# Performance work log

Measured on AMD Instinct MI355X. Metric: run time of the kernel, lower is better.

## Reference

```python
import jax, jax.numpy as jnp
import numpy as np

B, C_IN, T = 32, 192, 8192
H, N_PH, OUT = 192, 1024, 4
EPS = 1e-5


def setup_inputs() -> dict:
    key = jax.random.key(0)
    ks = jax.random.split(key, 12)
    s = 0.02
    return {
        "x": jax.random.normal(ks[0], (B, C_IN, T), jnp.float32),
        "x_mask": jnp.ones((B, 1, N_PH), jnp.float32),
        "w": jax.random.randint(ks[1], (B, 1, N_PH), 0, 8, jnp.int32),
        "pre_w": jax.random.normal(ks[2], (H, C_IN), jnp.float32) * s,
        "pre_b": jnp.zeros((H,), jnp.float32),
        "conv0_w": jax.random.normal(ks[3], (H, H, 3), jnp.float32) * s,
        "conv0_b": jnp.zeros((H,), jnp.float32),
        "ln0_g": jnp.ones((H,), jnp.float32),
        "ln0_b": jnp.zeros((H,), jnp.float32),
        "conv1_w": jax.random.normal(ks[4], (H, H, 3), jnp.float32) * s,
        "conv1_b": jnp.zeros((H,), jnp.float32),
        "ln1_g": jnp.ones((H,), jnp.float32),
        "ln1_b": jnp.zeros((H,), jnp.float32),
        "lin_w": jax.random.normal(ks[5], (OUT, H), jnp.float32) * s,
        "lin_b": jnp.zeros((OUT,), jnp.float32),
    }


def _segment_mean(x, w2):
    # x: [B, C, T] frames; w2: [B, n_ph] int durations.
    # Faithful to the torch double loop: phoneme j pools frames
    # [cumsum(w)[j-1] : cumsum(w)[j]); w==0 -> zeros.
    ends = jnp.cumsum(w2, axis=1)                      # [B, n_ph]
    t = jnp.arange(x.shape[2], dtype=ends.dtype)       # [T]
    ph_id = jax.vmap(lambda e: jnp.searchsorted(e, t, side="right"))(ends)  # [B, T]
    # segment sums over frames; extra segment n_ph catches out-of-range frames
    sums = jax.vmap(lambda xt, ids: jax.ops.segment_sum(xt, ids, num_segments=N_PH + 1))(
        x.transpose(0, 2, 1), ph_id
    )                                                  # [B, n_ph+1, C]
    sums = sums[:, :N_PH].transpose(0, 2, 1)           # [B, C, n_ph]
    denom = jnp.maximum(w2, 1).astype(x.dtype)[:, None, :]
    return jnp.where(w2[:, None, :] > 0, sums / denom, 0.0)


def _conv3(x, k, b):
    y = jax.lax.conv_general_dilated(x, k, (1,), [(1, 1)],
                                     dimension_numbers=("NCH", "OIH", "NCH"))
    return y + b[None, :, None]


def _ln(x, g, b):
    # channel-dim LayerNorm for [B, C, T] (VITS modules.LayerNorm)
    m = jnp.mean(x, axis=1, keepdims=True)
    v = jnp.mean(jnp.square(x - m), axis=1, keepdims=True)
    return (x - m) * jax.lax.rsqrt(v + EPS) * g[None, :, None] + b[None, :, None]


def reference(x, x_mask, w, pre_w, pre_b, conv0_w, conv0_b, ln0_g, ln0_b,
              conv1_w, conv1_b, ln1_g, ln1_b, lin_w, lin_b):
    w2 = w.reshape(w.shape[0], -1).astype(jnp.int32)
    spec = _segment_mean(x, w2)                                 # [B, C_in, n_ph]
    h = jnp.einsum("bct,hc->bht", spec, pre_w) + pre_b[None, :, None]
    # block 0: conv -> relu -> LN (dropout is identity at eval), mask before each layer
    h = _conv3(h * x_mask, conv0_w, conv0_b)
    h = jax.nn.relu(h * x_mask)
    h = _ln(h * x_mask, ln0_g, ln0_b)
    h = h * x_mask  # dropout(p=0.1) at eval = identity; mask still applied
    # block 1
    h = _conv3(h * x_mask, conv1_w, conv1_b)
    h = jax.nn.relu(h * x_mask)
    h = _ln(h * x_mask, ln1_g, ln1_b)
    h = h * x_mask
    p = jnp.einsum("bht,oh->bot", h, lin_w) + lin_b[None, :, None]
    return p * x_mask
```

## Files before the change

### kernel.cpp

```cpp
#include <hip/hip_runtime.h>
#include <hip/hip_bf16.h>

#define B 32
#define C_IN 192
#define T 8192
#define H 192
#define N_PH 1024
#define OUT 4
#define ROWP (2 * H)
#define HPITCH 392

typedef __attribute__((ext_vector_type(8))) short short8;
typedef __attribute__((ext_vector_type(4))) float f32x4;
typedef unsigned short ushort_t;

__device__ inline ushort_t f2bf(float f) {
    unsigned u = __builtin_bit_cast(unsigned, f);
    unsigned r = u + 0x7fffu + ((u >> 16) & 1u);
    return (ushort_t)(r >> 16);
}
__device__ inline float bf2f(ushort_t h) {
    unsigned u = ((unsigned)h) << 16;
    return __builtin_bit_cast(float, u);
}
__device__ inline void split_bf(float x, ushort_t& hi, ushort_t& lo) {
    hi = f2bf(x);
    lo = f2bf(x - bf2f(hi));
}

__device__ inline void wfrag_one(const float* __restrict__ w, ushort_t* __restrict__ wtf,
                                 int taps, int idx, int ntot) {
    int j  = idx & 7;
    int l  = (idx >> 3) & 63;
    int slot = idx >> 9;
    int nt = slot % 12;
    int ss = (slot / 12) % 6;
    int kt = slot / 72;
    int o  = nt * 16 + (l & 15);
    int i  = ss * 32 + ((l >> 4) << 3) + j;
    float v = (taps == 1) ? w[o * C_IN + i] : w[(o * H + i) * 3 + kt];
    ushort_t hi, lo;
    split_bf(v, hi, lo);
    wtf[idx] = hi;
    wtf[idx + ntot] = lo;
}

#define NWF 1008
__global__ __launch_bounds__(256) void prep_kernel(
    const float* __restrict__ pw, const float* __restrict__ w0,
    const float* __restrict__ w1, const int* __restrict__ wdur,
    ushort_t* __restrict__ wpre, ushort_t* __restrict__ w0t,
    ushort_t* __restrict__ w1t, int* __restrict__ ends)
{
    int blk = blockIdx.x;
    int tid = threadIdx.x;
    const int n1 = 36864, n3 = 110592;
    if (blk < NWF) {
        int idx = blk * 256 + tid;
        if (idx < n1) { wfrag_one(pw, wpre, 1, idx, n1); return; }
        idx -= n1;
        if (idx < n3) { wfrag_one(w0, w0t, 3, idx, n3); return; }
        idx -= n3;
        if (idx < n3) wfrag_one(w1, w1t, 3, idx, n3);
        return;
    }
    int b = blk - NWF;
    __shared__ int part[256];
    int4 w4 = ((const int4*)(wdur + b * N_PH))[tid];
    int c0 = w4.x, c1 = c0 + w4.y, c2 = c1 + w4.z, c3 = c2 + w4.w;
    part[tid] = c3;
    __syncthreads();
    for (int off = 1; off < 256; off <<= 1) {
        int v = (tid >= off) ? part[tid - off] : 0;
        __syncthreads();
        part[tid] += v;
        __syncthreads();
    }
    int pre = tid ? part[tid - 1] : 0;
    int4 e4;
    e4.x = pre + c0; e4.y = pre + c1; e4.z = pre + c2; e4.w = pre + c3;
    ((int4*)(ends + b * N_PH))[tid] = e4;
}

__global__ __launch_bounds__(256) void segmean_direct_kernel(
    const float* __restrict__ x, const int* __restrict__ ends,
    ushort_t* __restrict__ specT)
{
    int b  = blockIdx.x >> 5;
    int jt = (blockIdx.x & 31) * 32;
    int tid = threadIdx.x;
    int j_loc = tid & 31;
    int cg0 = tid >> 5;
    int j = jt + j_loc;

    __shared__ float sm[32][193];

    const int* eb = ends + b * N_PH;
    int e0 = eb[j];
    int s0 = j ? eb[j - 1] : 0;
    int len = e0 - s0;
    float inv = (len > 0) ? 1.f / (float)len : 0.f;

    const float* xb = x + (size_t)b * C_IN * T;
#pragma unroll 1
    for (int c = cg0; c < C_IN; c += 8) {
        const float* xr = xb + (size_t)c * T;
        float sum = 0.f;
        for (int t = s0; t < e0; ++t) sum += xr[t];
        sm[j_loc][c] = sum * inv;
    }
    __syncthreads();

    int r = tid >> 3;
    int g = tid & 7;
    ushort_t* ob = specT + ((size_t)b * N_PH + jt + r) * ROWP;
#pragma unroll
    for (int i0 = 0; i0 < 24; i0 += 8) {
        ushort_t th[8], tl[8];
#pragma unroll
        for (int k2 = 0; k2 < 8; ++k2) {
            int c = g * 24 + i0 + k2;
            split_bf(sm[r][c], th[k2], tl[k2]);
        }
        *(short8*)(ob + g * 24 + i0) = *(short8*)th;
        *(short8*)(ob + H + g * 24 + i0) = *(short8*)tl;
    }
}

__global__ __launch_bounds__(256) void chain_kernel(
    const ushort_t* __restrict__ specT,
    const ushort_t* __restrict__ wpre, const ushort_t* __restrict__ w0t,
    const ushort_t* __restrict__ w1t,
    const float* __restrict__ pre_b, const float* __restrict__ c0_b,
    const float* __restrict__ c1_b,
    const float* __restrict__ mask,
    const float* __restrict__ g0, const float* __restrict__ be0,
    const float* __restrict__ g1, const float* __restrict__ be1,
    const float* __restrict__ lw, const float* __restrict__ lb,
    float* __restrict__ out)
{
    const int b  = blockIdx.y;
    const int t0 = blockIdx.x * 64;
    const int tid = threadIdx.x;
    const int lane = tid & 63;
    const int wv = tid >> 6;
    const int nhalf = wv >> 1;
    const int mgrp = wv & 1;
    const int m = lane & 15;
    const int kg = (lane >> 4) << 3;
    const int rbase = (lane >> 4) << 2;

    __shared__ ushort_t hbuf[82 * HPITCH];
    __shared__ float g0_s[H], b0_s[H], g1_s[H], b1_s[H];
    __shared__ float lw_s[OUT * H];
    __shared__ float m_s[96], mstat[66], rstat[66];

    if (tid < H) { g0_s[tid] = g0[tid]; b0_s[tid] = be0[tid];
                   g1_s[tid] = g1[tid]; b1_s[tid] = be1[tid]; }
    if (tid < 96) {
        int grow = t0 - 2 + tid;
        m_s[tid] = (grow >= 0 && grow < N_PH) ? mask[b * N_PH + grow] : 0.f;
    }
    for (int i = tid; i < OUT * H; i += 256) lw_s[i] = lw[i];
    __syncthreads();

    const short8 z8 = {0, 0, 0, 0, 0, 0, 0, 0};

    {
        f32x4 acc[3][6];
#pragma unroll
        for (int n = 0; n < 6; ++n) {
            float bb = pre_b[(nhalf * 6 + n) * 16 + m];
#pragma unroll
            for (int f = 0; f < 3; ++f) acc[f][n] = (f32x4){bb, bb, bb, bb};
        }
        const ushort_t* inb = specT + (size_t)b * N_PH * ROWP;
#pragma unroll 1
        for (int s = 0; s < 6; ++s) {
            short8 ah[3], al[3], bh[6], bl[6];
#pragma unroll
            for (int f = 0; f < 3; ++f) {
                int trow = t0 - 2 + (mgrp * 3 + f) * 16 + m;
                if ((unsigned)trow < (unsigned)N_PH) {
                    const ushort_t* ar = inb + (size_t)trow * ROWP + s * 32 + kg;
                    ah[f] = *(const short8*)ar;
                    al[f] = *(const short8*)(ar + H);
                } else { ah[f] = z8; al[f] = z8; }
            }
            const ushort_t* wb = wpre + ((size_t)(s * 12 + nhalf * 6) << 9) + (lane << 3);
#pragma unroll
            for (int n = 0; n < 6; ++n) {
                bh[n] = *(const short8*)(wb + (n << 9));
                bl[n] = *(const short8*)(wb + (n << 9) + 36864);
            }
#pragma unroll
            for (int f = 0; f < 3; ++f)
#pragma unroll
                for (int n = 0; n < 6; ++n) {
                    acc[f][n] = __builtin_amdgcn_mfma_f32_16x16x32_bf16(ah[f], bh[n], acc[f][n], 0, 0, 0);
                    acc[f][n] = __builtin_amdgcn_mfma_f32_16x16x32_bf16(al[f], bh[n], acc[f][n], 0, 0, 0);
                    acc[f][n] = __builtin_amdgcn_mfma_f32_16x16x32_bf16(ah[f], bl[n], acc[f][n], 0, 0, 0);
                }
        }
#pragma unroll
        for (int f = 0; f < 3; ++f) {
            int lb0 = (mgrp * 3 + f) * 16 + rbase;
#pragma unroll
            for (int n = 0; n < 6; ++n) {
                int col = (nhalf * 6 + n) * 16 + m;
#pragma unroll
                for (int r = 0; r < 4; ++r) {
                    int l = lb0 + r;
                    if (l < 82) {
                        float v = acc[f][n][r] * m_s[l];
                        ushort_t hi, lo; split_bf(v, hi, lo);
                        hbuf[l * HPITCH + col] = hi;
                        hbuf[l * HPITCH + H + col] = lo;
                    }
                }
            }
        }
    }
    __syncthreads();

    {
        f32x4 acc[3][6];
        const int nf = mgrp ? 2 : 3;
        const int fbase = mgrp * 3;
#pragma unroll
        for (int n = 0; n < 6; ++n) {
            float bb = c0_b[(nhalf * 6 + n) * 16 + m];
#pragma unroll
            for (int f = 0; f < 3; ++f) acc[f][n] = (f32x4){bb, bb, bb, bb};
        }
#pragma unroll 1
        for (int kt = 0; kt < 3; ++kt)
#pragma unroll 1
            for (int s = 0; s < 6; ++s) {
                short8 ah[3], al[3], bh[6], bl[6];
#pragma unroll
                for (int f = 0; f < 3; ++f) {
                    if (f < nf) {
                        int l0 = (fbase + f) * 16 + m + kt;
                        const ushort_t* ar = hbuf + l0 * HPITCH + s * 32 + kg;
                        ah[f] = *(const short8*)ar;
                        al[f] = *(const short8*)(ar + H);
                    }
                }
                const ushort_t* wb = w0t + ((size_t)((kt * 6 + s) * 12 + nhalf * 6) << 9) + (lane << 3);
#pragma unroll
                for (int n = 0; n < 6; ++n) {
                    bh[n] = *(const short8*)(wb + (n << 9));
                    bl[n] = *(const short8*)(wb + (n << 9) + 110592);
                }
#pragma unroll
                for (int f = 0; f < 3; ++f) {
                    if (f < nf) {
#pragma unroll
                        for (int n = 0; n < 6; ++n) {
                            acc[f][n] = __builtin_amdgcn_mfma_f32_16x16x32_bf16(ah[f], bh[n], acc[f][n], 0, 0, 0);
                            acc[f][n] = __builtin_amdgcn_mfma_f32_16x16x32_bf16(al[f], bh[n], acc[f][n], 0, 0, 0);
                            acc[f][n] = __builtin_amdgcn_mfma_f32_16x16x32_bf16(ah[f], bl[n], acc[f][n], 0, 0, 0);
                        }
                    }
                }
            }
        __syncthreads();
#pragma unroll
        for (int f = 0; f < 3; ++f) {
            if (f < nf) {
                int lb1 = (fbase + f) * 16 + rbase;
#pragma unroll
                for (int n = 0; n < 6; ++n) {
                    int col = (nhalf * 6 + n) * 16 + m;
#pragma unroll
                    for (int r = 0; r < 4; ++r) {
                        int l = lb1 + r;
                        if (l < 66) {
                            float mm = m_s[l + 1];
                            float u = fmaxf(acc[f][n][r] * mm, 0.f) * mm;
                            ushort_t hi, lo; split_bf(u, hi, lo);
                            hbuf[l * HPITCH + col] = hi;
                            hbuf[l * HPITCH + H + col] = lo;
                        }
                    }
                }
            }
        }
    }
    __syncthreads();

    if (tid < 66) {
        float s = 0.f, ss = 0.f;
        for (int c = 0; c < H; ++c) {
            float v = bf2f(hbuf[tid * HPITCH + c]) + bf2f(hbuf[tid * HPITCH + H + c]);
            s += v; ss += v * v;
        }
        float mean = s * (1.f / (float)H);
        mstat[tid] = mean;
        rstat[tid] = rsqrtf(ss * (1.f / (float)H) - mean * mean + 1e-5f);
    }
    __syncthreads();
    for (int idx = tid; idx < 66 * H; idx += 256) {
        int row = idx / H;
        int c = idx - row * H;
        float v = bf2f(hbuf[row * HPITCH + c]) + bf2f(hbuf[row * HPITCH + H + c]);
        float mm = m_s[row + 1];
        float y = ((v - mstat[row]) * rstat[row] * g0_s[c] + b0_s[c]) * (mm * mm);
        ushort_t hi, lo; split_bf(y, hi, lo);
        hbuf[row * HPITCH + c] = hi;
        hbuf[row * HPITCH + H + c] = lo;
    }
    __syncthreads();

    {
        f32x4 acc[2][6];
#pragma unroll
        for (int n = 0; n < 6; ++n) {
            float bb = c1_b[(nhalf * 6 + n) * 16 + m];
            acc[0][n] = (f32x4){bb, bb, bb, bb};
            acc[1][n] = (f32x4){bb, bb, bb, bb};
        }
#pragma unroll 1
        for (int kt = 0; kt < 3; ++kt)
#pragma unroll 1
            for (int s = 0; s < 6; ++s) {
                short8 ah[2], al[2], bh[6], bl[6];
#pragma unroll
                for (int f = 0; f < 2; ++f) {
                    int l1 = (mgrp * 2 + f) * 16 + m + kt;
                    const ushort_t* ar = hbuf + l1 * HPITCH + s * 32 + kg;
                    ah[f] = *(const short8*)ar;
                    al[f] = *(const short8*)(ar + H);
                }
                const ushort_t* wb = w1t + ((size_t)((kt * 6 + s) * 12 + nhalf * 6) << 9) + (lane << 3);
#pragma unroll
                for (int n = 0; n < 6; ++n) {
                    bh[n] = *(const short8*)(wb + (n << 9));
                    bl[n] = *(const short8*)(wb + (n << 9) + 110592);
                }
#pragma unroll
                for (int f = 0; f < 2; ++f)
#pragma unroll
                    for (int n = 0; n < 6; ++n) {
                        acc[f][n] = __builtin_amdgcn_mfma_f32_16x16x32_bf16(ah[f], bh[n], acc[f][n], 0, 0, 0);
                        acc[f][n] = __builtin_amdgcn_mfma_f32_16x16x32_bf16(al[f], bh[n], acc[f][n], 0, 0, 0);
                        acc[f][n] = __builtin_amdgcn_mfma_f32_16x16x32_bf16(ah[f], bl[n], acc[f][n], 0, 0, 0);
                    }
            }
        __syncthreads();
#pragma unroll
        for (int f = 0; f < 2; ++f) {
            int lb2 = (mgrp * 2 + f) * 16 + rbase;
#pragma unroll
            for (int n = 0; n < 6; ++n) {
                int col = (nhalf * 6 + n) * 16 + m;
#pragma unroll
                for (int r = 0; r < 4; ++r) {
                    int l = lb2 + r;
                    float mm = m_s[l + 2];
                    float u = fmaxf(acc[f][n][r] * mm, 0.f) * mm;
                    ushort_t hi, lo; split_bf(u, hi, lo);
                    hbuf[l * HPITCH + col] = hi;
                    hbuf[l * HPITCH + H + col] = lo;
                }
            }
        }
    }
    __syncthreads();

    if (tid < 64) {
        float s = 0.f, ss = 0.f;
        for (int c = 0; c < H; ++c) {
            float v = bf2f(hbuf[tid * HPITCH + c]) + bf2f(hbuf[tid * HPITCH + H + c]);
            s += v; ss += v * v;
        }
        float mean = s * (1.f / (float)H);
        mstat[tid] = mean;
        rstat[tid] = rsqrtf(ss * (1.f / (float)H) - mean * mean + 1e-5f);
    }
    __syncthreads();

    {
        int row = tid >> 2;
        int q = tid & 3;
        float mean = mstat[row], rstd = rstat[row], mk = m_s[row + 2];
        float a0 = 0.f, a1 = 0.f, a2 = 0.f, a3 = 0.f;
#pragma unroll 1
        for (int c = q * 48; c < q * 48 + 48; ++c) {
            float v = bf2f(hbuf[row * HPITCH + c]) + bf2f(hbuf[row * HPITCH + H + c]);
            float y = ((v - mean) * rstd * g1_s[c] + b1_s[c]) * mk;
            a0 += lw_s[0 * H + c] * y;
            a1 += lw_s[1 * H + c] * y;
            a2 += lw_s[2 * H + c] * y;
            a3 += lw_s[3 * H + c] * y;
        }
        a0 += __shfl_xor(a0, 1); a0 += __shfl_xor(a0, 2);
        a1 += __shfl_xor(a1, 1); a1 += __shfl_xor(a1, 2);
        a2 += __shfl_xor(a2, 1); a2 += __shfl_xor(a2, 2);
        a3 += __shfl_xor(a3, 1); a3 += __shfl_xor(a3, 2);
        if (q == 0) {
            int t = t0 + row;
            float* ob = out + (size_t)b * OUT * N_PH + t;
            ob[0 * N_PH] = (a0 + lb[0]) * mk;
            ob[1 * N_PH] = (a1 + lb[1]) * mk;
            ob[2 * N_PH] = (a2 + lb[2]) * mk;
            ob[3 * N_PH] = (a3 + lb[3]) * mk;
        }
    }
}

extern "C" void kernel_launch(void* const* d_in, const int* in_sizes, int n_in,
                              void* d_out, int out_size, void* d_ws, size_t ws_size,
                              hipStream_t stream) {
    const float* x      = (const float*)d_in[0];
    const float* x_mask = (const float*)d_in[1];
    const int*   w      = (const int*)d_in[2];
    const float* pre_w  = (const float*)d_in[3];
    const float* pre_b  = (const float*)d_in[4];
    const float* conv0_w = (const float*)d_in[5];
    const float* conv0_b = (const float*)d_in[6];
    const float* ln0_g   = (const float*)d_in[7];
    const float* ln0_b   = (const float*)d_in[8];
    const float* conv1_w = (const float*)d_in[9];
    const float* conv1_b = (const float*)d_in[10];
    const float* ln1_g   = (const float*)d_in[11];
    const float* ln1_b   = (const float*)d_in[12];
    const float* lin_w   = (const float*)d_in[13];
    const float* lin_b   = (const float*)d_in[14];
    float* out = (float*)d_out;

    char* ws = (char*)d_ws;
    size_t off = 0;
    ushort_t* specT = (ushort_t*)(ws + off); off += (size_t)B * N_PH * ROWP * sizeof(ushort_t);
    ushort_t* wpre  = (ushort_t*)(ws + off); off += (size_t)2 * 36864 * sizeof(ushort_t);
    ushort_t* w0t   = (ushort_t*)(ws + off); off += (size_t)2 * 110592 * sizeof(ushort_t);
    ushort_t* w1t   = (ushort_t*)(ws + off); off += (size_t)2 * 110592 * sizeof(ushort_t);
    int* ends       = (int*)(ws + off);      off += (size_t)B * N_PH * sizeof(int);

    prep_kernel<<<NWF + B, 256, 0, stream>>>(pre_w, conv0_w, conv1_w, w,
                                             wpre, w0t, w1t, ends);

    segmean_direct_kernel<<<B * 32, 256, 0, stream>>>(x, ends, specT);

    chain_kernel<<<dim3(N_PH / 64, B), 256, 0, stream>>>(
        specT, wpre, w0t, w1t, pre_b, conv0_b, conv1_b, x_mask,
        ln0_g, ln0_b, ln1_g, ln1_b, lin_w, lin_b, out);
}
```

Measured before the change: 376.6 us.

## Shrink chain kernel tile to 32 phonemes and vectorize LayerNorm passes

The fused pre-projection/conv/LN chain kernel now processes 32 output positions per block instead of 64. This halves shared memory per block and doubles the grid, and launch bounds are set to allow 4 blocks per CU for occupancy. In exchange the 4-row halo recompute share grows, so more redundant MFMA work is done per output. The LayerNorm statistic and normalize passes are also rewritten to use all threads with 8-wide vector LDS loads and shuffle reductions. The final projection is split over 8 lanes per row.

```diff
diff --git a/kernel.cpp b/kernel.cpp
--- a/kernel.cpp
+++ b/kernel.cpp
@@ -9,6 +9,7 @@
 #define OUT 4
 #define ROWP (2 * H)
 #define HPITCH 392
+#define TILE 32
 
 typedef __attribute__((ext_vector_type(8))) short short8;
 typedef __attribute__((ext_vector_type(4))) float f32x4;
@@ -127,7 +128,7 @@
     }
 }
 
-__global__ __launch_bounds__(256) void chain_kernel(
+__global__ __launch_bounds__(256, 4) void chain_kernel(
     const ushort_t* __restrict__ specT,
     const ushort_t* __restrict__ wpre, const ushort_t* __restrict__ w0t,
     const ushort_t* __restrict__ w1t,
@@ -140,7 +141,7 @@
     float* __restrict__ out)
 {
     const int b  = blockIdx.y;
-    const int t0 = blockIdx.x * 64;
+    const int t0 = blockIdx.x * TILE;
     const int tid = threadIdx.x;
     const int lane = tid & 63;
     const int wv = tid >> 6;
@@ -150,14 +151,14 @@
     const int kg = (lane >> 4) << 3;
     const int rbase = (lane >> 4) << 2;
 
-    __shared__ ushort_t hbuf[82 * HPITCH];
+    __shared__ ushort_t hbuf[36 * HPITCH];
     __shared__ float g0_s[H], b0_s[H], g1_s[H], b1_s[H];
     __shared__ float lw_s[OUT * H];
-    __shared__ float m_s[96], mstat[66], rstat[66];
+    __shared__ float m_s[36], mstat[34], rstat[34];
 
     if (tid < H) { g0_s[tid] = g0[tid]; b0_s[tid] = be0[tid];
                    g1_s[tid] = g1[tid]; b1_s[tid] = be1[tid]; }
-    if (tid < 96) {
+    if (tid < 36) {
         int grow = t0 - 2 + tid;
         m_s[tid] = (grow >= 0 && grow < N_PH) ? mask[b * N_PH + grow] : 0.f;
     }
@@ -167,25 +168,29 @@
     const short8 z8 = {0, 0, 0, 0, 0, 0, 0, 0};
 
     {
-        f32x4 acc[3][6];
+        const int nf = mgrp ? 1 : 2;
+        f32x4 acc[2][6];
 #pragma unroll
         for (int n = 0; n < 6; ++n) {
             float bb = pre_b[(nhalf * 6 + n) * 16 + m];
-#pragma unroll
-            for (int f = 0; f < 3; ++f) acc[f][n] = (f32x4){bb, bb, bb, bb};
+            acc[0][n] = (f32x4){bb, bb, bb, bb};
+            acc[1][n] = (f32x4){bb, bb, bb, bb};
         }
         const ushort_t* inb = specT + (size_t)b * N_PH * ROWP;
 #pragma unroll 1
         for (int s = 0; s < 6; ++s) {
-            short8 ah[3], al[3], bh[6], bl[6];
-#pragma unroll
-            for (int f = 0; f < 3; ++f) {
-                int trow = t0 - 2 + (mgrp * 3 + f) * 16 + m;
-                if ((unsigned)trow < (unsigned)N_PH) {
-                    const ushort_t* ar = inb + (size_t)trow * ROWP + s * 32 + kg;
-                    ah[f] = *(const short8*)ar;
-                    al[f] = *(const short8*)(ar + H);
-                } else { ah[f] = z8; al[f] = z8; }
+            short8 ah[2], al[2], bh[6], bl[6];
+#pragma unroll
+            for (int f = 0; f < 2; ++f) {
+                if (f < nf) {
+                    int fb = mgrp ? 32 : f * 16;
+                    int trow = t0 - 2 + fb + m;
+                    if ((unsigned)trow < (unsigned)N_PH) {
+                        const ushort_t* ar = inb + (size_t)trow * ROWP + s * 32 + kg;
+                        ah[f] = *(const short8*)ar;
+                        al[f] = *(const short8*)(ar + H);
+                    } else { ah[f] = z8; al[f] = z8; }
+                }
             }
             const ushort_t* wb = wpre + ((size_t)(s * 12 + nhalf * 6) << 9) + (lane << 3);
 #pragma unroll
@@ -194,28 +199,33 @@
                 bl[n] = *(const short8*)(wb + (n << 9) + 36864);
             }
 #pragma unroll
-            for (int f = 0; f < 3; ++f)
+            for (int f = 0; f < 2; ++f) {
+                if (f < nf) {
+#pragma unroll
+                    for (int n = 0; n < 6; ++n) {
+                        acc[f][n] = __builtin_amdgcn_mfma_f32_16x16x32_bf16(ah[f], bh[n], acc[f][n], 0, 0, 0);
+                        acc[f][n] = __builtin_amdgcn_mfma_f32_16x16x32_bf16(al[f], bh[n], acc[f][n], 0, 0, 0);
+                        acc[f][n] = __builtin_amdgcn_mfma_f32_16x16x32_bf16(ah[f], bl[n], acc[f][n], 0, 0, 0);
+                    }
+                }
+            }
+        }
+#pragma unroll
+        for (int f = 0; f < 2; ++f) {
+            if (f < nf) {
+                int fb = mgrp ? 32 : f * 16;
 #pragma unroll
                 for (int n = 0; n < 6; ++n) {
-                    acc[f][n] = __builtin_amdgcn_mfma_f32_16x16x32_bf16(ah[f], bh[n], acc[f][n], 0, 0, 0);
-                    acc[f][n] = __builtin_amdgcn_mfma_f32_16x16x32_bf16(al[f], bh[n], acc[f][n], 0, 0, 0);
-                    acc[f][n] = __builtin_amdgcn_mfma_f32_16x16x32_bf16(ah[f], bl[n], acc[f][n], 0, 0, 0);
-                }
-        }
-#pragma unroll
-        for (int f = 0; f < 3; ++f) {
-            int lb0 = (mgrp * 3 + f) * 16 + rbase;
-#pragma unroll
-            for (int n = 0; n < 6; ++n) {
-                int col = (nhalf * 6 + n) * 16 + m;
-#pragma unroll
-                for (int r = 0; r < 4; ++r) {
-                    int l = lb0 + r;
-                    if (l < 82) {
-                        float v = acc[f][n][r] * m_s[l];
-                        ushort_t hi, lo; split_bf(v, hi, lo);
-                        hbuf[l * HPITCH + col] = hi;
-                        hbuf[l * HPITCH + H + col] = lo;
+                    int col = (nhalf * 6 + n) * 16 + m;
+#pragma unroll
+                    for (int r = 0; r < 4; ++r) {
+                        int l = fb + rbase + r;
+                        if (l < 36) {
+                            float v = acc[f][n][r] * m_s[l];
+                            ushort_t hi, lo; split_bf(v, hi, lo);
+                            hbuf[l * HPITCH + col] = hi;
+                            hbuf[l * HPITCH + H + col] = lo;
+                        }
                     }
                 }
             }
@@ -224,24 +234,24 @@
     __syncthreads();
 
     {
-        f32x4 acc[3][6];
-        const int nf = mgrp ? 2 : 3;
-        const int fbase = mgrp * 3;
+        const int nf = mgrp ? 1 : 2;
+        f32x4 acc[2][6];
 #pragma unroll
         for (int n = 0; n < 6; ++n) {
             float bb = c0_b[(nhalf * 6 + n) * 16 + m];
-#pragma unroll
-            for (int f = 0; f < 3; ++f) acc[f][n] = (f32x4){bb, bb, bb, bb};
+            acc[0][n] = (f32x4){bb, bb, bb, bb};
+            acc[1][n] = (f32x4){bb, bb, bb, bb};
         }
 #pragma unroll 1
         for (int kt = 0; kt < 3; ++kt)
 #pragma unroll 1
             for (int s = 0; s < 6; ++s) {
-                short8 ah[3], al[3], bh[6], bl[6];
-#pragma unroll
-                for (int f = 0; f < 3; ++f) {
+                short8 ah[2], al[2], bh[6], bl[6];
+#pragma unroll
+                for (int f = 0; f < 2; ++f) {
                     if (f < nf) {
-                        int l0 = (fbase + f) * 16 + m + kt;
+                        int fb = mgrp ? 18 : f * 16;
+                        int l0 = fb + m + kt;
                         const ushort_t* ar = hbuf + l0 * HPITCH + s * 32 + kg;
                         ah[f] = *(const short8*)ar;
                         al[f] = *(const short8*)(ar + H);
@@ -254,7 +264,7 @@
                     bl[n] = *(const short8*)(wb + (n << 9) + 110592);
                 }
 #pragma unroll
-                for (int f = 0; f < 3; ++f) {
+                for (int f = 0; f < 2; ++f) {
                     if (f < nf) {
 #pragma unroll
                         for (int n = 0; n < 6; ++n) {
@@ -267,21 +277,22 @@
             }
         __syncthreads();
 #pragma unroll
-        for (int f = 0; f < 3; ++f) {
+        for (int f = 0; f < 2; ++f) {
             if (f < nf) {
-                int lb1 = (fbase + f) * 16 + rbase;
+                int fb = mgrp ? 18 : f * 16;
 #pragma unroll
                 for (int n = 0; n < 6; ++n) {
                     int col = (nhalf * 6 + n) * 16 + m;
 #pragma unroll
                     for (int r = 0; r < 4; ++r) {
-                        int l = lb1 + r;
-                        if (l < 66) {
-                            float mm = m_s[l + 1];
+                        int l1 = fb + rbase + r;
+                        bool keep = mgrp ? (l1 >= 32 && l1 < 34) : true;
+                        if (keep) {
+                            float mm = m_s[l1 + 1];
                             float u = fmaxf(acc[f][n][r] * mm, 0.f) * mm;
                             ushort_t hi, lo; split_bf(u, hi, lo);
-                            hbuf[l * HPITCH + col] = hi;
-                            hbuf[l * HPITCH + H + col] = lo;
+                            hbuf[l1 * HPITCH + col] = hi;
+                            hbuf[l1 * HPITCH + H + col] = lo;
                         }
                     }
                 }
@@ -290,115 +301,151 @@
     }
     __syncthreads();
 
-    if (tid < 66) {
-        float s = 0.f, ss = 0.f;
-        for (int c = 0; c < H; ++c) {
-            float v = bf2f(hbuf[tid * HPITCH + c]) + bf2f(hbuf[tid * HPITCH + H + c]);
-            s += v; ss += v * v;
-        }
-        float mean = s * (1.f / (float)H);
-        mstat[tid] = mean;
-        rstat[tid] = rsqrtf(ss * (1.f / (float)H) - mean * mean + 1e-5f);
-    }
-    __syncthreads();
-    for (int idx = tid; idx < 66 * H; idx += 256) {
-        int row = idx / H;
-        int c = idx - row * H;
-        float v = bf2f(hbuf[row * HPITCH + c]) + bf2f(hbuf[row * HPITCH + H + c]);
+    {
+        int row = tid >> 2;
+        int q = tid & 3;
+        if (row < 34) {
+            float s = 0.f, ss = 0.f;
+#pragma unroll
+            for (int i = 0; i < 6; ++i) {
+                int c0 = q * 48 + i * 8;
+                short8 vh = *(const short8*)(hbuf + row * HPITCH + c0);
+                short8 vl = *(const short8*)(hbuf + row * HPITCH + H + c0);
+#pragma unroll
+                for (int k2 = 0; k2 < 8; ++k2) {
+                    float v = bf2f((ushort_t)vh[k2]) + bf2f((ushort_t)vl[k2]);
+                    s += v; ss += v * v;
+                }
+            }
+            s  += __shfl_xor(s, 1);  s  += __shfl_xor(s, 2);
+            ss += __shfl_xor(ss, 1); ss += __shfl_xor(ss, 2);
+            if (q == 0) {
+                float mean = s * (1.f / (float)H);
+                mstat[row] = mean;
+                rstat[row] = rsqrtf(ss * (1.f / (float)H) - mean * mean + 1e-5f);
+            }
+        }
+    }
+    __syncthreads();
+    for (int idx = tid; idx < 34 * 24; idx += 256) {
+        int row = idx / 24;
+        int c0 = (idx - row * 24) * 8;
+        float mean = mstat[row], rstd = rstat[row];
         float mm = m_s[row + 1];
-        float y = ((v - mstat[row]) * rstat[row] * g0_s[c] + b0_s[c]) * (mm * mm);
-        ushort_t hi, lo; split_bf(y, hi, lo);
-        hbuf[row * HPITCH + c] = hi;
-        hbuf[row * HPITCH + H + c] = lo;
-    }
-    __syncthreads();
-
-    {
-        f32x4 acc[2][6];
+        float mm2 = mm * mm;
+        short8 vh = *(const short8*)(hbuf + row * HPITCH + c0);
+        short8 vl = *(const short8*)(hbuf + row * HPITCH + H + c0);
+        ushort_t th[8], tl[8];
+#pragma unroll
+        for (int k2 = 0; k2 < 8; ++k2) {
+            int c = c0 + k2;
+            float v = bf2f((ushort_t)vh[k2]) + bf2f((ushort_t)vl[k2]);
+            float y = ((v - mean) * rstd * g0_s[c] + b0_s[c]) * mm2;
+            split_bf(y, th[k2], tl[k2]);
+        }
+        *(short8*)(hbuf + row * HPITCH + c0) = *(short8*)th;
+        *(short8*)(hbuf + row * HPITCH + H + c0) = *(short8*)tl;
+    }
+    __syncthreads();
+
+    {
+        f32x4 acc[6];
 #pragma unroll
         for (int n = 0; n < 6; ++n) {
             float bb = c1_b[(nhalf * 6 + n) * 16 + m];
-            acc[0][n] = (f32x4){bb, bb, bb, bb};
-            acc[1][n] = (f32x4){bb, bb, bb, bb};
+            acc[n] = (f32x4){bb, bb, bb, bb};
         }
 #pragma unroll 1
         for (int kt = 0; kt < 3; ++kt)
 #pragma unroll 1
             for (int s = 0; s < 6; ++s) {
-                short8 ah[2], al[2], bh[6], bl[6];
-#pragma unroll
-                for (int f = 0; f < 2; ++f) {
-                    int l1 = (mgrp * 2 + f) * 16 + m + kt;
-                    const ushort_t* ar = hbuf + l1 * HPITCH + s * 32 + kg;
-                    ah[f] = *(const short8*)ar;
-                    al[f] = *(const short8*)(ar + H);
-                }
+                int l1 = mgrp * 16 + m + kt;
+                const ushort_t* ar = hbuf + l1 * HPITCH + s * 32 + kg;
+                short8 ah = *(const short8*)ar;
+                short8 al = *(const short8*)(ar + H);
                 const ushort_t* wb = w1t + ((size_t)((kt * 6 + s) * 12 + nhalf * 6) << 9) + (lane << 3);
+                short8 bh[6], bl[6];
 #pragma unroll
                 for (int n = 0; n < 6; ++n) {
                     bh[n] = *(const short8*)(wb + (n << 9));
                     bl[n] = *(const short8*)(wb + (n << 9) + 110592);
                 }
 #pragma unroll
-                for (int f = 0; f < 2; ++f)
-#pragma unroll
-                    for (int n = 0; n < 6; ++n) {
-                        acc[f][n] = __builtin_amdgcn_mfma_f32_16x16x32_bf16(ah[f], bh[n], acc[f][n], 0, 0, 0);
-                        acc[f][n] = __builtin_amdgcn_mfma_f32_16x16x32_bf16(al[f], bh[n], acc[f][n], 0, 0, 0);
-                        acc[f][n] = __builtin_amdgcn_mfma_f32_16x16x32_bf16(ah[f], bl[n], acc[f][n], 0, 0, 0);
-                    }
+                for (int n = 0; n < 6; ++n) {
+                    acc[n] = __builtin_amdgcn_mfma_f32_16x16x32_bf16(ah, bh[n], acc[n], 0, 0, 0);
+                    acc[n] = __builtin_amdgcn_mfma_f32_16x16x32_bf16(al, bh[n], acc[n], 0, 0, 0);
+                    acc[n] = __builtin_amdgcn_mfma_f32_16x16x32_bf16(ah, bl[n], acc[n], 0, 0, 0);
+                }
             }
         __syncthreads();
 #pragma unroll
-        for (int f = 0; f < 2; ++f) {
-            int lb2 = (mgrp * 2 + f) * 16 + rbase;
-#pragma unroll
-            for (int n = 0; n < 6; ++n) {
-                int col = (nhalf * 6 + n) * 16 + m;
-#pragma unroll
-                for (int r = 0; r < 4; ++r) {
-                    int l = lb2 + r;
-                    float mm = m_s[l + 2];
-                    float u = fmaxf(acc[f][n][r] * mm, 0.f) * mm;
-                    ushort_t hi, lo; split_bf(u, hi, lo);
-                    hbuf[l * HPITCH + col] = hi;
-                    hbuf[l * HPITCH + H + col] = lo;
-                }
-            }
-        }
-    }
-    __syncthreads();
-
-    if (tid < 64) {
-        float s = 0.f, ss = 0.f;
-        for (int c = 0; c < H; ++c) {
-            float v = bf2f(hbuf[tid * HPITCH + c]) + bf2f(hbuf[tid * HPITCH + H + c]);
-            s += v; ss += v * v;
-        }
-        float mean = s * (1.f / (float)H);
-        mstat[tid] = mean;
-        rstat[tid] = rsqrtf(ss * (1.f / (float)H) - mean * mean + 1e-5f);
+        for (int n = 0; n < 6; ++n) {
+            int col = (nhalf * 6 + n) * 16 + m;
+#pragma unroll
+            for (int r = 0; r < 4; ++r) {
+                int l2 = mgrp * 16 + rbase + r;
+                float mm = m_s[l2 + 2];
+                float u = fmaxf(acc[n][r] * mm, 0.f) * mm;
+                ushort_t hi, lo; split_bf(u, hi, lo);
+                hbuf[l2 * HPITCH + col] = hi;
+                hbuf[l2 * HPITCH + H + col] = lo;
+            }
+        }
     }
     __syncthreads();
 
     {
         int row = tid >> 2;
         int q = tid & 3;
+        if (row < 32) {
+            float s = 0.f, ss = 0.f;
+#pragma unroll
+            for (int i = 0; i < 6; ++i) {
+                int c0 = q * 48 + i * 8;
+                short8 vh = *(const short8*)(hbuf + row * HPITCH + c0);
+                short8 vl = *(const short8*)(hbuf + row * HPITCH + H + c0);
+#pragma unroll
+                for (int k2 = 0; k2 < 8; ++k2) {
+                    float v = bf2f((ushort_t)vh[k2]) + bf2f((ushort_t)vl[k2]);
+                    s += v; ss += v * v;
+                }
+            }
+            s  += __shfl_xor(s, 1);  s  += __shfl_xor(s, 2);
+            ss += __shfl_xor(ss, 1); ss += __shfl_xor(ss, 2);
+            if (q == 0) {
+                float mean = s * (1.f / (float)H);
+                mstat[row] = mean;
+                rstat[row] = rsqrtf(ss * (1.f / (float)H) - mean * mean + 1e-5f);
+            }
+        }
+    }
+    __syncthreads();
+
+    {
+        int row = tid >> 3;
+        int q = tid & 7;
         float mean = mstat[row], rstd = rstat[row], mk = m_s[row + 2];
         float a0 = 0.f, a1 = 0.f, a2 = 0.f, a3 = 0.f;
-#pragma unroll 1
-        for (int c = q * 48; c < q * 48 + 48; ++c) {
-            float v = bf2f(hbuf[row * HPITCH + c]) + bf2f(hbuf[row * HPITCH + H + c]);
-            float y = ((v - mean) * rstd * g1_s[c] + b1_s[c]) * mk;
-            a0 += lw_s[0 * H + c] * y;
-            a1 += lw_s[1 * H + c] * y;
-            a2 += lw_s[2 * H + c] * y;
-            a3 += lw_s[3 * H + c] * y;
-        }
-        a0 += __shfl_xor(a0, 1); a0 += __shfl_xor(a0, 2);
-        a1 += __shfl_xor(a1, 1); a1 += __shfl_xor(a1, 2);
-        a2 += __shfl_xor(a2, 1); a2 += __shfl_xor(a2, 2);
-        a3 += __shfl_xor(a3, 1); a3 += __shfl_xor(a3, 2);
+#pragma unroll
+        for (int i = 0; i < 3; ++i) {
+            int c0 = q * 24 + i * 8;
+            short8 vh = *(const short8*)(hbuf + row * HPITCH + c0);
+            short8 vl = *(const short8*)(hbuf + row * HPITCH + H + c0);
+#pragma unroll
+            for (int k2 = 0; k2 < 8; ++k2) {
+                int c = c0 + k2;
+                float v = bf2f((ushort_t)vh[k2]) + bf2f((ushort_t)vl[k2]);
+                float y = ((v - mean) * rstd * g1_s[c] + b1_s[c]) * mk;
+                a0 += lw_s[0 * H + c] * y;
+                a1 += lw_s[1 * H + c] * y;
+                a2 += lw_s[2 * H + c] * y;
+                a3 += lw_s[3 * H + c] * y;
+            }
+        }
+        a0 += __shfl_xor(a0, 1); a0 += __shfl_xor(a0, 2); a0 += __shfl_xor(a0, 4);
+        a1 += __shfl_xor(a1, 1); a1 += __shfl_xor(a1, 2); a1 += __shfl_xor(a1, 4);
+        a2 += __shfl_xor(a2, 1); a2 += __shfl_xor(a2, 2); a2 += __shfl_xor(a2, 4);
+        a3 += __shfl_xor(a3, 1); a3 += __shfl_xor(a3, 2); a3 += __shfl_xor(a3, 4);
         if (q == 0) {
             int t = t0 + row;
             float* ob = out + (size_t)b * OUT * N_PH + t;
@@ -443,7 +490,7 @@
 
     segmean_direct_kernel<<<B * 32, 256, 0, stream>>>(x, ends, specT);
 
-    chain_kernel<<<dim3(N_PH / 64, B), 256, 0, stream>>>(
+    chain_kernel<<<dim3(N_PH / TILE, B), 256, 0, stream>>>(
         specT, wpre, w0t, w1t, pre_b, conv0_b, conv1_b, x_mask,
         ln0_g, ln0_b, ln1_g, ln1_b, lin_w, lin_b, out);
 }
```

New measurement: 376.5 us. About the same (-0.0%).
